# Kernel optimization log

Measured on AMD Instinct MI355X. Metric: run time of the kernel, lower is better.

## Reference

```python
import jax, jax.numpy as jnp
import numpy as np
import math
from jax import lax

VOCAB = 32000
D = 128          # embedding_dim
S = 512          # seq_len == input_channels
B = 8
HID = 512        # hidden_size
NBUCK = 32       # n_buckets
NHYP = 5         # log2(n_buckets)
ENCODERS = 2
OUT = 6
EPS = 1e-5


def _positional_encoding(max_len, d):
    pos = np.arange(max_len, dtype=np.float32)[:, None]
    div = np.exp(np.arange(0, d, 2, dtype=np.float32) * (-math.log(10000.0) / d))
    pe = np.zeros((max_len, d), dtype=np.float32)
    pe[:, 0::2] = np.sin(pos * div)
    pe[:, 1::2] = np.cos(pos * div)
    return jnp.asarray(pe)


def setup_inputs() -> dict:
    key = jax.random.key(0)
    ks = jax.random.split(key, 10)
    emb = jax.random.normal(ks[0], (VOCAB, D), jnp.float32)
    emb = emb.at[VOCAB - 1].set(0.0)  # padding_idx row is zero in torch
    sc = 0.05
    return {
        "inputs": jax.random.randint(ks[1], (B, S), 0, VOCAB - 1),
        "emb": emb,
        # Faithful quirk: pe is indexed by x.size(0)=batch, so only pe[:B] is used.
        "pe": _positional_encoding(B, D),               # [B, D]
        "hyperplanes": jax.random.normal(ks[2], (D + 1, NHYP), jnp.float32),
        "Wq": jax.random.normal(ks[3], (D, D), jnp.float32) * sc,
        "bq": jnp.zeros((D,), jnp.float32),
        "Wv": jax.random.normal(ks[4], (D, D), jnp.float32) * sc,
        "bv": jnp.zeros((D,), jnp.float32),
        "ln_g": jnp.ones((D,), jnp.float32),
        "ln_b": jnp.zeros((D,), jnp.float32),
        "W1": jax.random.normal(ks[5], (D, HID), jnp.float32) * sc,
        "b1": jnp.zeros((HID,), jnp.float32),
        "W2": jax.random.normal(ks[6], (HID, D), jnp.float32) * sc,
        "b2": jnp.zeros((D,), jnp.float32),
        "Wm": jax.random.normal(ks[7], (S * D, OUT), jnp.float32) * 0.01,
        "bm": jnp.zeros((OUT,), jnp.float32),
    }


def _layernorm(x, g, b):
    mu = jnp.mean(x, axis=-1, keepdims=True)
    var = jnp.mean(jnp.square(x - mu), axis=-1, keepdims=True)
    return (x - mu) * lax.rsqrt(var + EPS) * g + b


def _lsh_attention(x, Wq, bq, Wv, bv, hyperplanes):
    q = x @ Wq + bq                                      # [B,S,D]
    v = x @ Wv + bv                                      # [B,S,D]
    # LSH bucket ids from q (hard threshold -> no grad through buckets)
    qh = jnp.concatenate([q, jnp.ones(q.shape[:-1] + (1,), q.dtype)], axis=-1)
    proj = jnp.einsum('bse,en->bsn', qh, hyperplanes)    # [B,S,NHYP]
    bits = (proj >= 0).astype(jnp.float32)
    pow2 = 2.0 ** jnp.arange(NHYP, dtype=jnp.float32)
    buckets = jnp.einsum('bsn,n->bs', bits, pow2).astype(jnp.int32)  # [B,S]
    scale = 1.0 / math.sqrt(D)

    def step(acc, i):
        # Faithful quirk: masked_fill zeros tokens IN bucket i (inverted mask).
        keep = (buckets != i)[..., None]                 # [B,S,1]
        qb = jnp.where(keep, q, 0.0)
        vb = jnp.where(keep, v, 0.0)
        att = jax.nn.softmax(jnp.einsum('bsd,btd->bst', qb, qb) * scale, axis=-1)
        return acc + jnp.einsum('bst,btd->bsd', att, vb), None

    out, _ = lax.scan(step, jnp.zeros_like(x), jnp.arange(NBUCK))
    return out


def reference(inputs, emb, pe, hyperplanes, Wq, bq, Wv, bv, ln_g, ln_b,
              W1, b1, W2, b2, Wm, bm):
    x = emb[inputs]                                      # [B,S,D]
    x = x + pe[:, None, :]                               # broadcast over seq (faithful quirk)
    for _ in range(ENCODERS):
        a = _lsh_attention(x, Wq, bq, Wv, bv, hyperplanes)
        x = _layernorm(a, ln_g, ln_b)
        x = (jax.nn.relu(x @ W1 + b1) @ W2 + b2) + x     # fc residual (dropout=eval)
        x = _layernorm(x, ln_g, ln_b)
    x = x.reshape(x.shape[0], -1)                        # [B, S*D]
    return x @ Wm + bm                                   # [B, OUT]
```

## Files before the change

### kernel.cpp

```cpp
#include <hip/hip_runtime.h>
#include <hip/hip_bf16.h>

#define BB   8
#define SS   512
#define DD   128
#define HH   512
#define NBK  32


__global__ void k_embed(const int* __restrict__ idx, const float* __restrict__ emb,
                        const float* __restrict__ pe, float* __restrict__ x) {
    int b = blockIdx.x;
    int t = b * 16384 + blockIdx.y * 256 + threadIdx.x;
    int tok = t >> 5, d4 = (t & 31) * 4;
    float4 ev = *(const float4*)&emb[(size_t)idx[tok] * DD + d4];
    float4 pv = *(const float4*)&pe[b * DD + d4];
    ev.x += pv.x; ev.y += pv.y; ev.z += pv.z; ev.w += pv.w;
    *(float4*)&x[(size_t)tok * DD + d4] = ev;
}

__global__ __launch_bounds__(256) void k_qvb(const float* __restrict__ x,
        const float* __restrict__ Wq, const float* __restrict__ bq,
        const float* __restrict__ Wv, const float* __restrict__ bv,
        const float* __restrict__ hyp,
        float* __restrict__ q, float* __restrict__ v, float* __restrict__ qT,
        int* __restrict__ bucket) {
    int rb = blockIdx.x * 32 + blockIdx.y;
    __shared__ __align__(16) float xs[16][132];
    __shared__ float qts[128][17];
    int tid = threadIdx.x;
    #pragma unroll
    for (int it = 0; it < 2; ++it) {
        int lin = tid + 256 * it;
        int r = lin >> 5, kq = (lin & 31) * 4;
        *(float4*)&xs[r][kq] = *(const float4*)&x[(size_t)(rb * 16 + r) * DD + kq];
    }
    __syncthreads();
    int tx = tid & 63;
    int ty = tid >> 6;
    float2 aq[4], av[4];
    #pragma unroll
    for (int i = 0; i < 4; ++i) { aq[i] = make_float2(0.f, 0.f); av[i] = make_float2(0.f, 0.f); }
    for (int g = 0; g < 32; ++g) {
        int kb = g * 4;
        float4 a0 = *(const float4*)&xs[ty * 4 + 0][kb];
        float4 a1 = *(const float4*)&xs[ty * 4 + 1][kb];
        float4 a2 = *(const float4*)&xs[ty * 4 + 2][kb];
        float4 a3 = *(const float4*)&xs[ty * 4 + 3][kb];
        #pragma unroll
        for (int j = 0; j < 4; ++j) {
            float2 wq = *(const float2*)&Wq[(size_t)(kb + j) * DD + tx * 2];
            float2 wv = *(const float2*)&Wv[(size_t)(kb + j) * DD + tx * 2];
            float c0 = (j == 0) ? a0.x : (j == 1) ? a0.y : (j == 2) ? a0.z : a0.w;
            float c1 = (j == 0) ? a1.x : (j == 1) ? a1.y : (j == 2) ? a1.z : a1.w;
            float c2 = (j == 0) ? a2.x : (j == 1) ? a2.y : (j == 2) ? a2.z : a2.w;
            float c3 = (j == 0) ? a3.x : (j == 1) ? a3.y : (j == 2) ? a3.z : a3.w;
            aq[0].x += c0 * wq.x; aq[0].y += c0 * wq.y; av[0].x += c0 * wv.x; av[0].y += c0 * wv.y;
            aq[1].x += c1 * wq.x; aq[1].y += c1 * wq.y; av[1].x += c1 * wv.x; av[1].y += c1 * wv.y;
            aq[2].x += c2 * wq.x; aq[2].y += c2 * wq.y; av[2].x += c2 * wv.x; av[2].y += c2 * wv.y;
            aq[3].x += c3 * wq.x; aq[3].y += c3 * wq.y; av[3].x += c3 * wv.x; av[3].y += c3 * wv.y;
        }
    }
    float2 bqv = *(const float2*)&bq[tx * 2];
    float2 bvv = *(const float2*)&bv[tx * 2];
    float2 oq[4], ov[4];
    #pragma unroll
    for (int i = 0; i < 4; ++i) {
        oq[i] = make_float2(aq[i].x + bqv.x, aq[i].y + bqv.y);
        ov[i] = make_float2(av[i].x + bvv.x, av[i].y + bvv.y);
        int row = rb * 16 + ty * 4 + i;
        *(float2*)&q[(size_t)row * DD + tx * 2] = oq[i];
        *(float2*)&v[(size_t)row * DD + tx * 2] = ov[i];
        qts[2 * tx][ty * 4 + i]     = oq[i].x;
        qts[2 * tx + 1][ty * 4 + i] = oq[i].y;
    }
    float h0[5], h1[5];
    #pragma unroll
    for (int h = 0; h < 5; ++h) {
        h0[h] = hyp[(2 * tx) * 5 + h];
        h1[h] = hyp[(2 * tx + 1) * 5 + h];
    }
    float pr[4][5];
    #pragma unroll
    for (int r = 0; r < 4; ++r)
        #pragma unroll
        for (int h = 0; h < 5; ++h)
            pr[r][h] = oq[r].x * h0[h] + oq[r].y * h1[h];
    #pragma unroll
    for (int o = 1; o < 64; o <<= 1)
        #pragma unroll
        for (int r = 0; r < 4; ++r)
            #pragma unroll
            for (int h = 0; h < 5; ++h)
                pr[r][h] += __shfl_xor(pr[r][h], o, 64);
    if (tx == 0) {
        #pragma unroll
        for (int r = 0; r < 4; ++r) {
            int bb = 0;
            #pragma unroll
            for (int h = 0; h < 5; ++h)
                if (pr[r][h] + hyp[128 * 5 + h] >= 0.f) bb |= (1 << h);
            bucket[rb * 16 + ty * 4 + r] = bb;
        }
    }
    __syncthreads();
    {
        int b  = blockIdx.x;
        int t0 = blockIdx.y * 16;
        int k  = tid >> 1, o = (tid & 1) * 8;
        float4 v0 = make_float4(qts[k][o], qts[k][o + 1], qts[k][o + 2], qts[k][o + 3]);
        float4 v1 = make_float4(qts[k][o + 4], qts[k][o + 5], qts[k][o + 6], qts[k][o + 7]);
        size_t base = ((size_t)b * DD + k) * SS + t0 + o;
        *(float4*)&qT[base]     = v0;
        *(float4*)&qT[base + 4] = v1;
    }
}

__global__ __launch_bounds__(256) void k_vb(const float* __restrict__ v,
        const int* __restrict__ bucket, float* __restrict__ Vb,
        int* __restrict__ cnt) {
    int b  = blockIdx.x;
    int bk = blockIdx.y;
    int tid = threadIdx.x;
    __shared__ int bkt_sh[512];
    __shared__ float red[128];
    bkt_sh[tid]       = bucket[b * SS + tid];
    bkt_sh[tid + 256] = bucket[b * SS + tid + 256];
    __syncthreads();
    int d = tid & 127, half = tid >> 7;
    const float* vbp = v + (size_t)b * SS * DD + d;
    float acc = 0.f;
    #pragma unroll 8
    for (int i = 0; i < 256; ++i) {
        int tok = half * 256 + i;
        float val = vbp[(size_t)tok * DD];
        acc += (bkt_sh[tok] == bk) ? val : 0.f;
    }
    if (half == 1) red[d] = acc;
    __syncthreads();
    if (half == 0)
        Vb[(size_t)((b << 5) + bk) * DD + d] = acc + red[d];
    if (tid < 64) {
        int c = 0;
        #pragma unroll
        for (int i = 0; i < 8; ++i) c += (bkt_sh[tid * 8 + i] == bk) ? 1 : 0;
        #pragma unroll
        for (int o = 1; o < 64; o <<= 1) c += __shfl_xor(c, o, 64);
        if (tid == 0) cnt[(b << 5) + bk] = c;
    }
}

__global__ __launch_bounds__(256) void k_gattn(const float* __restrict__ qT,
        const float* __restrict__ q, const float* __restrict__ v,
        const int* __restrict__ bucket, const int* __restrict__ cnt,
        const float* __restrict__ Vb,
        const float* __restrict__ g, const float* __restrict__ lb,
        float* __restrict__ x) {
    int bz = blockIdx.x, s0 = blockIdx.y * 16;
    int tid = threadIdx.x;
    __shared__ __align__(16) float qs[16][132];
    __shared__ __align__(16) float cs[16][528];
    __shared__ __align__(16) float osh[16][132];
    __shared__ int   bkt[512];
    __shared__ float Wsh[16][32];
    __shared__ float rsh[16][32];
    __shared__ float Zsh[16], Rsh[16], Msh[16];
    __shared__ float cntf[32];
    __shared__ int   bssh[16];
    #pragma unroll
    for (int it = 0; it < 2; ++it) {
        int lin = tid + 256 * it;
        int r = lin >> 5, kq = (lin & 31) * 4;
        *(float4*)&qs[r][kq] = *(const float4*)&q[(size_t)(bz * SS + s0 + r) * DD + kq];
    }
    bkt[tid]       = bucket[bz * SS + tid];
    bkt[tid + 256] = bucket[bz * SS + tid + 256];
    if (tid < 32) cntf[tid] = (float)cnt[(bz << 5) + tid];
    if (tid < 16) bssh[tid] = bucket[bz * SS + s0 + tid];
    __syncthreads();
    const float scale = 0.088388347648318447f;
    {
        int kh = tid >> 7;
        int ty = (tid >> 5) & 3;
        int txg = tid & 31;
        for (int cc = 0; cc < 4; ++cc) {
            float4 acc[4];
            #pragma unroll
            for (int i = 0; i < 4; ++i) acc[i] = make_float4(0.f, 0.f, 0.f, 0.f);
            const float* qtb = qT + ((size_t)bz * DD + kh * 64) * SS + cc * 128 + txg * 4;
            for (int gg = 0; gg < 16; ++gg) {
                int kb = kh * 64 + gg * 4;
                float4 a0 = *(const float4*)&qs[ty * 4 + 0][kb];
                float4 a1 = *(const float4*)&qs[ty * 4 + 1][kb];
                float4 a2 = *(const float4*)&qs[ty * 4 + 2][kb];
                float4 a3 = *(const float4*)&qs[ty * 4 + 3][kb];
                #pragma unroll
                for (int j = 0; j < 4; ++j) {
                    float4 b4 = *(const float4*)&qtb[(size_t)(gg * 4 + j) * SS];
                    float c0 = (j == 0) ? a0.x : (j == 1) ? a0.y : (j == 2) ? a0.z : a0.w;
                    float c1 = (j == 0) ? a1.x : (j == 1) ? a1.y : (j == 2) ? a1.z : a1.w;
                    float c2 = (j == 0) ? a2.x : (j == 1) ? a2.y : (j == 2) ? a2.z : a2.w;
                    float c3 = (j == 0) ? a3.x : (j == 1) ? a3.y : (j == 2) ? a3.z : a3.w;
                    acc[0].x += c0 * b4.x; acc[0].y += c0 * b4.y; acc[0].z += c0 * b4.z; acc[0].w += c0 * b4.w;
                    acc[1].x += c1 * b4.x; acc[1].y += c1 * b4.y; acc[1].z += c1 * b4.z; acc[1].w += c1 * b4.w;
                    acc[2].x += c2 * b4.x; acc[2].y += c2 * b4.y; acc[2].z += c2 * b4.z; acc[2].w += c2 * b4.w;
                    acc[3].x += c3 * b4.x; acc[3].y += c3 * b4.y; acc[3].z += c3 * b4.z; acc[3].w += c3 * b4.w;
                }
            }
            if (kh == 1) {
                #pragma unroll
                for (int i = 0; i < 4; ++i)
                    *(float4*)&cs[ty * 4 + i][cc * 128 + txg * 4] = acc[i];
            }
            __syncthreads();
            if (kh == 0) {
                #pragma unroll
                for (int i = 0; i < 4; ++i) {
                    float4 p = *(const float4*)&cs[ty * 4 + i][cc * 128 + txg * 4];
                    p.x = (p.x + acc[i].x) * scale;
                    p.y = (p.y + acc[i].y) * scale;
                    p.z = (p.z + acc[i].z) * scale;
                    p.w = (p.w + acc[i].w) * scale;
                    *(float4*)&cs[ty * 4 + i][cc * 128 + txg * 4] = p;
                }
            }
            __syncthreads();
        }
    }
    int row = tid >> 4, l = tid & 15;
    {
        float m = 0.f;
        #pragma unroll 8
        for (int i = 0; i < 32; ++i) m = fmaxf(m, cs[row][l + 16 * i]);
        #pragma unroll
        for (int o = 1; o < 16; o <<= 1) m = fmaxf(m, __shfl_xor(m, o, 16));
        if (l == 0) Msh[row] = m;
        Wsh[row][l * 2] = 0.f; Wsh[row][l * 2 + 1] = 0.f;
    }
    __syncthreads();
    {
        float Ms = Msh[row];
        #pragma unroll 8
        for (int i = 0; i < 32; ++i) {
            int c = l + 16 * i;
            float ev = __expf(cs[row][c] - Ms);
            cs[row][c] = ev;
            atomicAdd(&Wsh[row][bkt[c]], ev);
        }
    }
    __syncthreads();
    if (tid < 16) {
        float z = 0.f;
        #pragma unroll
        for (int i = 0; i < NBK; ++i) z += Wsh[tid][i];
        Zsh[tid] = z;
    }
    __syncthreads();
    #pragma unroll
    for (int j = 0; j < 2; ++j) {
        int p = tid + 256 * j;
        int r = p >> 5, bkid = p & 31;
        rsh[r][bkid] = 1.0f / (Zsh[r] - Wsh[r][bkid] + cntf[bkid] * __expf(-Msh[r]));
    }
    __syncthreads();
    if (tid < 16) {
        int bs = bssh[tid];
        float R = 0.f;
        #pragma unroll
        for (int i = 0; i < NBK; ++i) R += (i == bs) ? 0.f : rsh[tid][i];
        Rsh[tid] = R;
    }
    __syncthreads();
    {
        float R = Rsh[row];
        int bs = bssh[row];
        #pragma unroll 8
        for (int i = 0; i < 32; ++i) {
            int c = l + 16 * i;
            int bc = bkt[c];
            float rsel = (bc == bs) ? 0.f : rsh[row][bc];
            cs[row][c] *= (R - rsel);
        }
    }
    __syncthreads();
    {
        int kh = tid >> 7;
        int ty = (tid >> 5) & 3;
        int tx = tid & 31;
        float4 acc[4];
        #pragma unroll
        for (int i = 0; i < 4; ++i) acc[i] = make_float4(0.f, 0.f, 0.f, 0.f);
        const float* vb_base = v + (size_t)bz * SS * DD + tx * 4;
        for (int gg = 0; gg < 64; ++gg) {
            int kb = kh * 256 + gg * 4;
            float4 a0 = *(const float4*)&cs[ty * 4 + 0][kb];
            float4 a1 = *(const float4*)&cs[ty * 4 + 1][kb];
            float4 a2 = *(const float4*)&cs[ty * 4 + 2][kb];
            float4 a3 = *(const float4*)&cs[ty * 4 + 3][kb];
            #pragma unroll
            for (int j = 0; j < 4; ++j) {
                float4 vj = *(const float4*)&vb_base[(size_t)(kb + j) * DD];
                float c0 = (j == 0) ? a0.x : (j == 1) ? a0.y : (j == 2) ? a0.z : a0.w;
                float c1 = (j == 0) ? a1.x : (j == 1) ? a1.y : (j == 2) ? a1.z : a1.w;
                float c2 = (j == 0) ? a2.x : (j == 1) ? a2.y : (j == 2) ? a2.z : a2.w;
                float c3 = (j == 0) ? a3.x : (j == 1) ? a3.y : (j == 2) ? a3.z : a3.w;
                acc[0].x += c0 * vj.x; acc[0].y += c0 * vj.y; acc[0].z += c0 * vj.z; acc[0].w += c0 * vj.w;
                acc[1].x += c1 * vj.x; acc[1].y += c1 * vj.y; acc[1].z += c1 * vj.z; acc[1].w += c1 * vj.w;
                acc[2].x += c2 * vj.x; acc[2].y += c2 * vj.y; acc[2].z += c2 * vj.z; acc[2].w += c2 * vj.w;
                acc[3].x += c3 * vj.x; acc[3].y += c3 * vj.y; acc[3].z += c3 * vj.z; acc[3].w += c3 * vj.w;
            }
        }
        if (kh == 1) {
            #pragma unroll
            for (int i = 0; i < 4; ++i)
                *(float4*)&osh[ty * 4 + i][tx * 4] = acc[i];
        }
        __syncthreads();
        if (kh == 0) {
            float4 vs = make_float4(0.f, 0.f, 0.f, 0.f);
            #pragma unroll
            for (int i = 0; i < NBK; ++i) {
                float4 t = *(const float4*)&Vb[(size_t)((bz << 5) + i) * DD + tx * 4];
                vs.x += t.x; vs.y += t.y; vs.z += t.z; vs.w += t.w;
            }
            const float inv512 = 1.0f / 512.0f;
            #pragma unroll
            for (int i = 0; i < 4; ++i) {
                int r = ty * 4 + i;
                int bs = bssh[r];
                float4 vb4 = *(const float4*)&Vb[(size_t)((bz << 5) + bs) * DD + tx * 4];
                float4 p = *(const float4*)&osh[r][tx * 4];
                p.x += acc[i].x + (vs.x - vb4.x) * inv512;
                p.y += acc[i].y + (vs.y - vb4.y) * inv512;
                p.z += acc[i].z + (vs.z - vb4.z) * inv512;
                p.w += acc[i].w + (vs.w - vb4.w) * inv512;
                *(float4*)&osh[r][tx * 4] = p;
            }
        }
    }
    __syncthreads();
    {
        int r = tid >> 4, ll = tid & 15;
        float4 v0 = *(const float4*)&osh[r][ll * 8];
        float4 v1 = *(const float4*)&osh[r][ll * 8 + 4];
        float s  = v0.x + v0.y + v0.z + v0.w + v1.x + v1.y + v1.z + v1.w;
        float ss = v0.x*v0.x + v0.y*v0.y + v0.z*v0.z + v0.w*v0.w
                 + v1.x*v1.x + v1.y*v1.y + v1.z*v1.z + v1.w*v1.w;
        #pragma unroll
        for (int o = 1; o < 16; o <<= 1) {
            s  += __shfl_xor(s, o, 16);
            ss += __shfl_xor(ss, o, 16);
        }
        float mean = s * (1.f / 128.f);
        float var = ss * (1.f / 128.f) - mean * mean;
        float rstd = rsqrtf(var + 1e-5f);
        float4 g0 = *(const float4*)&g[ll * 8];
        float4 g1 = *(const float4*)&g[ll * 8 + 4];
        float4 b0 = *(const float4*)&lb[ll * 8];
        float4 b1v = *(const float4*)&lb[ll * 8 + 4];
        float4 o0, o1;
        o0.x = (v0.x - mean) * rstd * g0.x + b0.x;
        o0.y = (v0.y - mean) * rstd * g0.y + b0.y;
        o0.z = (v0.z - mean) * rstd * g0.z + b0.z;
        o0.w = (v0.w - mean) * rstd * g0.w + b0.w;
        o1.x = (v1.x - mean) * rstd * g1.x + b1v.x;
        o1.y = (v1.y - mean) * rstd * g1.y + b1v.y;
        o1.z = (v1.z - mean) * rstd * g1.z + b1v.z;
        o1.w = (v1.w - mean) * rstd * g1.w + b1v.w;
        size_t base = (size_t)(bz * SS + s0 + r) * DD + ll * 8;
        *(float4*)&x[base]     = o0;
        *(float4*)&x[base + 4] = o1;
    }
}

__global__ __launch_bounds__(512) void k_ffn(const float* __restrict__ x,
        const float* __restrict__ W1, const float* __restrict__ b1,
        const float* __restrict__ W2, const float* __restrict__ b2,
        const float* __restrict__ g, const float* __restrict__ lb,
        float* __restrict__ xout) {
    int rb = blockIdx.x * 32 + blockIdx.y;
    int tid = threadIdx.x;
    __shared__ __align__(16) float xs[16][132];
    __shared__ __align__(16) float hs[16][520];
    __shared__ __align__(16) float osh[16][132];
    {
        int r = tid >> 5, kq = (tid & 31) * 4;
        *(float4*)&xs[r][kq] = *(const float4*)&x[(size_t)(rb * 16 + r) * DD + kq];
    }
    __syncthreads();
    {
        int tx = tid & 127, ty = tid >> 7;
        float4 acc[4];
        #pragma unroll
        for (int i = 0; i < 4; ++i) acc[i] = make_float4(0.f, 0.f, 0.f, 0.f);
        for (int gg = 0; gg < 32; ++gg) {
            int kb = gg * 4;
            float4 a0 = *(const float4*)&xs[ty * 4 + 0][kb];
            float4 a1 = *(const float4*)&xs[ty * 4 + 1][kb];
            float4 a2 = *(const float4*)&xs[ty * 4 + 2][kb];
            float4 a3 = *(const float4*)&xs[ty * 4 + 3][kb];
            #pragma unroll
            for (int j = 0; j < 4; ++j) {
                float4 w = *(const float4*)&W1[(size_t)(kb + j) * HH + tx * 4];
                float c0 = (j == 0) ? a0.x : (j == 1) ? a0.y : (j == 2) ? a0.z : a0.w;
                float c1 = (j == 0) ? a1.x : (j == 1) ? a1.y : (j == 2) ? a1.z : a1.w;
                float c2 = (j == 0) ? a2.x : (j == 1) ? a2.y : (j == 2) ? a2.z : a2.w;
                float c3 = (j == 0) ? a3.x : (j == 1) ? a3.y : (j == 2) ? a3.z : a3.w;
                acc[0].x += c0 * w.x; acc[0].y += c0 * w.y; acc[0].z += c0 * w.z; acc[0].w += c0 * w.w;
                acc[1].x += c1 * w.x; acc[1].y += c1 * w.y; acc[1].z += c1 * w.z; acc[1].w += c1 * w.w;
                acc[2].x += c2 * w.x; acc[2].y += c2 * w.y; acc[2].z += c2 * w.z; acc[2].w += c2 * w.w;
                acc[3].x += c3 * w.x; acc[3].y += c3 * w.y; acc[3].z += c3 * w.z; acc[3].w += c3 * w.w;
            }
        }
        float4 bi = *(const float4*)&b1[tx * 4];
        #pragma unroll
        for (int i = 0; i < 4; ++i) {
            float4 hv;
            hv.x = fmaxf(acc[i].x + bi.x, 0.f);
            hv.y = fmaxf(acc[i].y + bi.y, 0.f);
            hv.z = fmaxf(acc[i].z + bi.z, 0.f);
            hv.w = fmaxf(acc[i].w + bi.w, 0.f);
            *(float4*)&hs[ty * 4 + i][tx * 4] = hv;
        }
    }
    __syncthreads();
    {
        int kh = tid >> 7;
        int ty = (tid >> 5) & 3;
        int tx = tid & 31;
        float4 acc[4];
        #pragma unroll
        for (int i = 0; i < 4; ++i) acc[i] = make_float4(0.f, 0.f, 0.f, 0.f);
        for (int gg = 0; gg < 32; ++gg) {
            int kb = kh * 128 + gg * 4;
            float4 a0 = *(const float4*)&hs[ty * 4 + 0][kb];
            float4 a1 = *(const float4*)&hs[ty * 4 + 1][kb];
            float4 a2 = *(const float4*)&hs[ty * 4 + 2][kb];
            float4 a3 = *(const float4*)&hs[ty * 4 + 3][kb];
            #pragma unroll
            for (int j = 0; j < 4; ++j) {
                float4 w = *(const float4*)&W2[(size_t)(kb + j) * DD + tx * 4];
                float c0 = (j == 0) ? a0.x : (j == 1) ? a0.y : (j == 2) ? a0.z : a0.w;
                float c1 = (j == 0) ? a1.x : (j == 1) ? a1.y : (j == 2) ? a1.z : a1.w;
                float c2 = (j == 0) ? a2.x : (j == 1) ? a2.y : (j == 2) ? a2.z : a2.w;
                float c3 = (j == 0) ? a3.x : (j == 1) ? a3.y : (j == 2) ? a3.z : a3.w;
                acc[0].x += c0 * w.x; acc[0].y += c0 * w.y; acc[0].z += c0 * w.z; acc[0].w += c0 * w.w;
                acc[1].x += c1 * w.x; acc[1].y += c1 * w.y; acc[1].z += c1 * w.z; acc[1].w += c1 * w.w;
                acc[2].x += c2 * w.x; acc[2].y += c2 * w.y; acc[2].z += c2 * w.z; acc[2].w += c2 * w.w;
                acc[3].x += c3 * w.x; acc[3].y += c3 * w.y; acc[3].z += c3 * w.z; acc[3].w += c3 * w.w;
            }
        }
        if (kh == 0) {
            float4 bi = *(const float4*)&b2[tx * 4];
            #pragma unroll
            for (int i = 0; i < 4; ++i) {
                int r = ty * 4 + i;
                float4 res = *(const float4*)&xs[r][tx * 4];
                float4 o;
                o.x = acc[i].x + bi.x + res.x;
                o.y = acc[i].y + bi.y + res.y;
                o.z = acc[i].z + bi.z + res.z;
                o.w = acc[i].w + bi.w + res.w;
                *(float4*)&osh[r][tx * 4] = o;
            }
        }
        __syncthreads();
        #pragma unroll
        for (int p = 1; p < 4; ++p) {
            if (kh == p) {
                #pragma unroll
                for (int i = 0; i < 4; ++i) {
                    int r = ty * 4 + i;
                    float4 o = *(const float4*)&osh[r][tx * 4];
                    o.x += acc[i].x; o.y += acc[i].y; o.z += acc[i].z; o.w += acc[i].w;
                    *(float4*)&osh[r][tx * 4] = o;
                }
            }
            __syncthreads();
        }
    }
    int row = tid >> 5, l = tid & 31;
    float4 val = *(const float4*)&osh[row][l * 4];
    float s = val.x + val.y + val.z + val.w;
    float ss = val.x * val.x + val.y * val.y + val.z * val.z + val.w * val.w;
    #pragma unroll
    for (int o = 1; o < 32; o <<= 1) {
        s  += __shfl_xor(s, o, 32);
        ss += __shfl_xor(ss, o, 32);
    }
    float mean = s * (1.f / 128.f);
    float var = ss * (1.f / 128.f) - mean * mean;
    float rstd = rsqrtf(var + 1e-5f);
    float4 gv = *(const float4*)&g[l * 4];
    float4 bv = *(const float4*)&lb[l * 4];
    float4 out;
    out.x = (val.x - mean) * rstd * gv.x + bv.x;
    out.y = (val.y - mean) * rstd * gv.y + bv.y;
    out.z = (val.z - mean) * rstd * gv.z + bv.z;
    out.w = (val.w - mean) * rstd * gv.w + bv.w;
    *(float4*)&xout[(size_t)(rb * 16 + row) * DD + l * 4] = out;
}

__global__ __launch_bounds__(256) void k_final(const float* __restrict__ x,
        const float* __restrict__ Wm, const float* __restrict__ bm,
        float* __restrict__ out) {
    int b = blockIdx.x >> 5, chunk = blockIdx.x & 31;
    int tid = threadIdx.x;
    const float* xr = x + (size_t)b * 65536 + chunk * 2048;
    const float* wr = Wm + (size_t)(chunk * 2048) * 6;
    float p[6] = {0.f, 0.f, 0.f, 0.f, 0.f, 0.f};
    #pragma unroll
    for (int it = 0; it < 8; ++it) {
        int j = tid + 256 * it;
        float xv = xr[j];
        const float* w = wr + (size_t)j * 6;
        p[0] += xv * w[0]; p[1] += xv * w[1]; p[2] += xv * w[2];
        p[3] += xv * w[3]; p[4] += xv * w[4]; p[5] += xv * w[5];
    }
    #pragma unroll
    for (int o = 0; o < 6; ++o)
        #pragma unroll
        for (int off = 1; off < 64; off <<= 1)
            p[o] += __shfl_xor(p[o], off, 64);
    __shared__ float red[4][6];
    int wv = tid >> 6;
    if ((tid & 63) == 0)
        #pragma unroll
        for (int o = 0; o < 6; ++o) red[wv][o] = p[o];
    __syncthreads();
    if (tid < 6) {
        float sv = red[0][tid] + red[1][tid] + red[2][tid] + red[3][tid];
        if (chunk == 0) sv += bm[tid];
        atomicAdd(&out[b * 6 + tid], sv);
    }
}

extern "C" void kernel_launch(void* const* d_in, const int* in_sizes, int n_in,
                              void* d_out, int out_size, void* d_ws, size_t ws_size,
                              hipStream_t stream) {
    const int*   inputs = (const int*)  d_in[0];
    const float* emb    = (const float*)d_in[1];
    const float* pe     = (const float*)d_in[2];
    const float* hyp    = (const float*)d_in[3];
    const float* Wq     = (const float*)d_in[4];
    const float* bq     = (const float*)d_in[5];
    const float* Wv     = (const float*)d_in[6];
    const float* bv     = (const float*)d_in[7];
    const float* ln_g   = (const float*)d_in[8];
    const float* ln_b   = (const float*)d_in[9];
    const float* W1     = (const float*)d_in[10];
    const float* b1     = (const float*)d_in[11];
    const float* W2     = (const float*)d_in[12];
    const float* b2     = (const float*)d_in[13];
    const float* Wm     = (const float*)d_in[14];
    const float* bm     = (const float*)d_in[15];

    float* F = (float*)d_ws;
    float* x     = F + 0;
    float* q     = F + 524288;
    float* v     = F + 1048576;
    float* qT    = F + 1572864;
    float* Vb    = F + 2097152;
    int*   cnt   = (int*)(F + 2129920);
    int*   bucket= (int*)(F + 2130176);

    hipMemsetAsync(d_out, 0, (size_t)out_size * 4, stream);
    k_embed<<<dim3(8, 64), 256, 0, stream>>>(inputs, emb, pe, x);

    for (int enc = 0; enc < 2; ++enc) {
        k_qvb<<<dim3(8, 32), 256, 0, stream>>>(x, Wq, bq, Wv, bv, hyp, q, v, qT, bucket);
        k_vb<<<dim3(8, 32), 256, 0, stream>>>(v, bucket, Vb, cnt);
        k_gattn<<<dim3(8, 32), 256, 0, stream>>>(qT, q, v, bucket, cnt, Vb, ln_g, ln_b, x);
        k_ffn<<<dim3(8, 32), 512, 0, stream>>>(x, W1, b1, W2, b2, ln_g, ln_b, x);
    }
    k_final<<<48 * 32 / 6, 256, 0, stream>>>(x, Wm, bm, (float*)d_out);
}
```

Baseline: 284.3 us.

## Double k_gattn block to 512 threads and repartition score and PV work

The grouped attention kernel now runs 512 threads per block instead of 256. In the QK^T stage each thread group owns one 128-column chunk over the full K=128, which removes the serial cc loop and the split-K reduction with its syncs. The softmax and layernorm stages map one 32-lane group to each row. The PV product is split four ways over K with a staged shared-memory reduction. This adds more parallelism per block for a grid of only 256 blocks, at the cost of extra reduction syncs and possibly higher register pressure.

```diff
diff --git a/kernel.cpp b/kernel.cpp
--- a/kernel.cpp
+++ b/kernel.cpp
@@ -150,7 +150,7 @@
     }
 }
 
-__global__ __launch_bounds__(256) void k_gattn(const float* __restrict__ qT,
+__global__ __launch_bounds__(512) void k_gattn(const float* __restrict__ qT,
         const float* __restrict__ q, const float* __restrict__ v,
         const int* __restrict__ bucket, const int* __restrict__ cnt,
         const float* __restrict__ Vb,
@@ -167,82 +167,67 @@
     __shared__ float Zsh[16], Rsh[16], Msh[16];
     __shared__ float cntf[32];
     __shared__ int   bssh[16];
-    #pragma unroll
-    for (int it = 0; it < 2; ++it) {
-        int lin = tid + 256 * it;
-        int r = lin >> 5, kq = (lin & 31) * 4;
+    {
+        int r = tid >> 5, kq = (tid & 31) * 4;
         *(float4*)&qs[r][kq] = *(const float4*)&q[(size_t)(bz * SS + s0 + r) * DD + kq];
     }
-    bkt[tid]       = bucket[bz * SS + tid];
-    bkt[tid + 256] = bucket[bz * SS + tid + 256];
+    bkt[tid] = bucket[bz * SS + tid];
     if (tid < 32) cntf[tid] = (float)cnt[(bz << 5) + tid];
     if (tid < 16) bssh[tid] = bucket[bz * SS + s0 + tid];
     __syncthreads();
     const float scale = 0.088388347648318447f;
     {
-        int kh = tid >> 7;
-        int ty = (tid >> 5) & 3;
+        int cc  = tid >> 7;
+        int ty  = (tid >> 5) & 3;
         int txg = tid & 31;
-        for (int cc = 0; cc < 4; ++cc) {
-            float4 acc[4];
-            #pragma unroll
-            for (int i = 0; i < 4; ++i) acc[i] = make_float4(0.f, 0.f, 0.f, 0.f);
-            const float* qtb = qT + ((size_t)bz * DD + kh * 64) * SS + cc * 128 + txg * 4;
-            for (int gg = 0; gg < 16; ++gg) {
-                int kb = kh * 64 + gg * 4;
-                float4 a0 = *(const float4*)&qs[ty * 4 + 0][kb];
-                float4 a1 = *(const float4*)&qs[ty * 4 + 1][kb];
-                float4 a2 = *(const float4*)&qs[ty * 4 + 2][kb];
-                float4 a3 = *(const float4*)&qs[ty * 4 + 3][kb];
-                #pragma unroll
-                for (int j = 0; j < 4; ++j) {
-                    float4 b4 = *(const float4*)&qtb[(size_t)(gg * 4 + j) * SS];
-                    float c0 = (j == 0) ? a0.x : (j == 1) ? a0.y : (j == 2) ? a0.z : a0.w;
-                    float c1 = (j == 0) ? a1.x : (j == 1) ? a1.y : (j == 2) ? a1.z : a1.w;
-                    float c2 = (j == 0) ? a2.x : (j == 1) ? a2.y : (j == 2) ? a2.z : a2.w;
-                    float c3 = (j == 0) ? a3.x : (j == 1) ? a3.y : (j == 2) ? a3.z : a3.w;
-                    acc[0].x += c0 * b4.x; acc[0].y += c0 * b4.y; acc[0].z += c0 * b4.z; acc[0].w += c0 * b4.w;
-                    acc[1].x += c1 * b4.x; acc[1].y += c1 * b4.y; acc[1].z += c1 * b4.z; acc[1].w += c1 * b4.w;
-                    acc[2].x += c2 * b4.x; acc[2].y += c2 * b4.y; acc[2].z += c2 * b4.z; acc[2].w += c2 * b4.w;
-                    acc[3].x += c3 * b4.x; acc[3].y += c3 * b4.y; acc[3].z += c3 * b4.z; acc[3].w += c3 * b4.w;
-                }
-            }
-            if (kh == 1) {
-                #pragma unroll
-                for (int i = 0; i < 4; ++i)
-                    *(float4*)&cs[ty * 4 + i][cc * 128 + txg * 4] = acc[i];
-            }
-            __syncthreads();
-            if (kh == 0) {
-                #pragma unroll
-                for (int i = 0; i < 4; ++i) {
-                    float4 p = *(const float4*)&cs[ty * 4 + i][cc * 128 + txg * 4];
-                    p.x = (p.x + acc[i].x) * scale;
-                    p.y = (p.y + acc[i].y) * scale;
-                    p.z = (p.z + acc[i].z) * scale;
-                    p.w = (p.w + acc[i].w) * scale;
-                    *(float4*)&cs[ty * 4 + i][cc * 128 + txg * 4] = p;
-                }
-            }
-            __syncthreads();
-        }
-    }
-    int row = tid >> 4, l = tid & 15;
+        float4 acc[4];
+        #pragma unroll
+        for (int i = 0; i < 4; ++i) acc[i] = make_float4(0.f, 0.f, 0.f, 0.f);
+        const float* qtb = qT + (size_t)bz * DD * SS + cc * 128 + txg * 4;
+        for (int gg = 0; gg < 32; ++gg) {
+            int kb = gg * 4;
+            float4 a0 = *(const float4*)&qs[ty * 4 + 0][kb];
+            float4 a1 = *(const float4*)&qs[ty * 4 + 1][kb];
+            float4 a2 = *(const float4*)&qs[ty * 4 + 2][kb];
+            float4 a3 = *(const float4*)&qs[ty * 4 + 3][kb];
+            #pragma unroll
+            for (int j = 0; j < 4; ++j) {
+                float4 b4 = *(const float4*)&qtb[(size_t)(kb + j) * SS];
+                float c0 = (j == 0) ? a0.x : (j == 1) ? a0.y : (j == 2) ? a0.z : a0.w;
+                float c1 = (j == 0) ? a1.x : (j == 1) ? a1.y : (j == 2) ? a1.z : a1.w;
+                float c2 = (j == 0) ? a2.x : (j == 1) ? a2.y : (j == 2) ? a2.z : a2.w;
+                float c3 = (j == 0) ? a3.x : (j == 1) ? a3.y : (j == 2) ? a3.z : a3.w;
+                acc[0].x += c0 * b4.x; acc[0].y += c0 * b4.y; acc[0].z += c0 * b4.z; acc[0].w += c0 * b4.w;
+                acc[1].x += c1 * b4.x; acc[1].y += c1 * b4.y; acc[1].z += c1 * b4.z; acc[1].w += c1 * b4.w;
+                acc[2].x += c2 * b4.x; acc[2].y += c2 * b4.y; acc[2].z += c2 * b4.z; acc[2].w += c2 * b4.w;
+                acc[3].x += c3 * b4.x; acc[3].y += c3 * b4.y; acc[3].z += c3 * b4.z; acc[3].w += c3 * b4.w;
+            }
+        }
+        #pragma unroll
+        for (int i = 0; i < 4; ++i) {
+            float4 p;
+            p.x = acc[i].x * scale; p.y = acc[i].y * scale;
+            p.z = acc[i].z * scale; p.w = acc[i].w * scale;
+            *(float4*)&cs[ty * 4 + i][cc * 128 + txg * 4] = p;
+        }
+    }
+    __syncthreads();
+    int row = tid >> 5, l = tid & 31;
     {
         float m = 0.f;
-        #pragma unroll 8
-        for (int i = 0; i < 32; ++i) m = fmaxf(m, cs[row][l + 16 * i]);
-        #pragma unroll
-        for (int o = 1; o < 16; o <<= 1) m = fmaxf(m, __shfl_xor(m, o, 16));
+        #pragma unroll
+        for (int i = 0; i < 16; ++i) m = fmaxf(m, cs[row][l + 32 * i]);
+        #pragma unroll
+        for (int o = 1; o < 32; o <<= 1) m = fmaxf(m, __shfl_xor(m, o, 32));
         if (l == 0) Msh[row] = m;
-        Wsh[row][l * 2] = 0.f; Wsh[row][l * 2 + 1] = 0.f;
+        Wsh[row][l] = 0.f;
     }
     __syncthreads();
     {
         float Ms = Msh[row];
-        #pragma unroll 8
-        for (int i = 0; i < 32; ++i) {
-            int c = l + 16 * i;
+        #pragma unroll
+        for (int i = 0; i < 16; ++i) {
+            int c = l + 32 * i;
             float ev = __expf(cs[row][c] - Ms);
             cs[row][c] = ev;
             atomicAdd(&Wsh[row][bkt[c]], ev);
@@ -256,12 +241,7 @@
         Zsh[tid] = z;
     }
     __syncthreads();
-    #pragma unroll
-    for (int j = 0; j < 2; ++j) {
-        int p = tid + 256 * j;
-        int r = p >> 5, bkid = p & 31;
-        rsh[r][bkid] = 1.0f / (Zsh[r] - Wsh[r][bkid] + cntf[bkid] * __expf(-Msh[r]));
-    }
+    rsh[row][l] = 1.0f / (Zsh[row] - Wsh[row][l] + cntf[l] * __expf(-Msh[row]));
     __syncthreads();
     if (tid < 16) {
         int bs = bssh[tid];
@@ -274,9 +254,9 @@
     {
         float R = Rsh[row];
         int bs = bssh[row];
-        #pragma unroll 8
-        for (int i = 0; i < 32; ++i) {
-            int c = l + 16 * i;
+        #pragma unroll
+        for (int i = 0; i < 16; ++i) {
+            int c = l + 32 * i;
             int bc = bkt[c];
             float rsel = (bc == bs) ? 0.f : rsh[row][bc];
             cs[row][c] *= (R - rsel);
@@ -291,8 +271,8 @@
         #pragma unroll
         for (int i = 0; i < 4; ++i) acc[i] = make_float4(0.f, 0.f, 0.f, 0.f);
         const float* vb_base = v + (size_t)bz * SS * DD + tx * 4;
-        for (int gg = 0; gg < 64; ++gg) {
-            int kb = kh * 256 + gg * 4;
+        for (int gg = 0; gg < 32; ++gg) {
+            int kb = kh * 128 + gg * 4;
             float4 a0 = *(const float4*)&cs[ty * 4 + 0][kb];
             float4 a1 = *(const float4*)&cs[ty * 4 + 1][kb];
             float4 a2 = *(const float4*)&cs[ty * 4 + 2][kb];
@@ -310,12 +290,25 @@
                 acc[3].x += c3 * vj.x; acc[3].y += c3 * vj.y; acc[3].z += c3 * vj.z; acc[3].w += c3 * vj.w;
             }
         }
-        if (kh == 1) {
+        if (kh == 3) {
             #pragma unroll
             for (int i = 0; i < 4; ++i)
                 *(float4*)&osh[ty * 4 + i][tx * 4] = acc[i];
         }
         __syncthreads();
+        #pragma unroll
+        for (int p = 2; p >= 1; --p) {
+            if (kh == p) {
+                #pragma unroll
+                for (int i = 0; i < 4; ++i) {
+                    int r = ty * 4 + i;
+                    float4 o = *(const float4*)&osh[r][tx * 4];
+                    o.x += acc[i].x; o.y += acc[i].y; o.z += acc[i].z; o.w += acc[i].w;
+                    *(float4*)&osh[r][tx * 4] = o;
+                }
+            }
+            __syncthreads();
+        }
         if (kh == 0) {
             float4 vs = make_float4(0.f, 0.f, 0.f, 0.f);
             #pragma unroll
@@ -340,36 +333,25 @@
     }
     __syncthreads();
     {
-        int r = tid >> 4, ll = tid & 15;
-        float4 v0 = *(const float4*)&osh[r][ll * 8];
-        float4 v1 = *(const float4*)&osh[r][ll * 8 + 4];
-        float s  = v0.x + v0.y + v0.z + v0.w + v1.x + v1.y + v1.z + v1.w;
-        float ss = v0.x*v0.x + v0.y*v0.y + v0.z*v0.z + v0.w*v0.w
-                 + v1.x*v1.x + v1.y*v1.y + v1.z*v1.z + v1.w*v1.w;
-        #pragma unroll
-        for (int o = 1; o < 16; o <<= 1) {
-            s  += __shfl_xor(s, o, 16);
-            ss += __shfl_xor(ss, o, 16);
+        float4 val = *(const float4*)&osh[row][l * 4];
+        float s = val.x + val.y + val.z + val.w;
+        float ss = val.x * val.x + val.y * val.y + val.z * val.z + val.w * val.w;
+        #pragma unroll
+        for (int o = 1; o < 32; o <<= 1) {
+            s  += __shfl_xor(s, o, 32);
+            ss += __shfl_xor(ss, o, 32);
         }
         float mean = s * (1.f / 128.f);
         float var = ss * (1.f / 128.f) - mean * mean;
         float rstd = rsqrtf(var + 1e-5f);
-        float4 g0 = *(const float4*)&g[ll * 8];
-        float4 g1 = *(const float4*)&g[ll * 8 + 4];
-        float4 b0 = *(const float4*)&lb[ll * 8];
-        float4 b1v = *(const float4*)&lb[ll * 8 + 4];
-        float4 o0, o1;
-        o0.x = (v0.x - mean) * rstd * g0.x + b0.x;
-        o0.y = (v0.y - mean) * rstd * g0.y + b0.y;
-        o0.z = (v0.z - mean) * rstd * g0.z + b0.z;
-        o0.w = (v0.w - mean) * rstd * g0.w + b0.w;
-        o1.x = (v1.x - mean) * rstd * g1.x + b1v.x;
-        o1.y = (v1.y - mean) * rstd * g1.y + b1v.y;
-        o1.z = (v1.z - mean) * rstd * g1.z + b1v.z;
-        o1.w = (v1.w - mean) * rstd * g1.w + b1v.w;
-        size_t base = (size_t)(bz * SS + s0 + r) * DD + ll * 8;
-        *(float4*)&x[base]     = o0;
-        *(float4*)&x[base + 4] = o1;
+        float4 gv = *(const float4*)&g[l * 4];
+        float4 bv = *(const float4*)&lb[l * 4];
+        float4 out;
+        out.x = (val.x - mean) * rstd * gv.x + bv.x;
+        out.y = (val.y - mean) * rstd * gv.y + bv.y;
+        out.z = (val.z - mean) * rstd * gv.z + bv.z;
+        out.w = (val.w - mean) * rstd * gv.w + bv.w;
+        *(float4*)&x[(size_t)(bz * SS + s0 + row) * DD + l * 4] = out;
     }
 }
 
@@ -570,7 +552,7 @@
     for (int enc = 0; enc < 2; ++enc) {
         k_qvb<<<dim3(8, 32), 256, 0, stream>>>(x, Wq, bq, Wv, bv, hyp, q, v, qT, bucket);
         k_vb<<<dim3(8, 32), 256, 0, stream>>>(v, bucket, Vb, cnt);
-        k_gattn<<<dim3(8, 32), 256, 0, stream>>>(qT, q, v, bucket, cnt, Vb, ln_g, ln_b, x);
+        k_gattn<<<dim3(8, 32), 512, 0, stream>>>(qT, q, v, bucket, cnt, Vb, ln_g, ln_b, x);
         k_ffn<<<dim3(8, 32), 512, 0, stream>>>(x, W1, b1, W2, b2, ln_g, ln_b, x);
     }
     k_final<<<48 * 32 / 6, 256, 0, stream>>>(x, Wm, bm, (float*)d_out);
```

Measured after the change: 262.5 us. -7.7%, faster.
